# Kernel optimization log

Hardware: AMD Instinct MI355X
Metric: run time of the kernel (lower is better)

## Reference

```python
import jax, jax.numpy as jnp
import numpy as np

N = 100000
E = 1600000
D_IN = 64
D_HID = 64
D_OUT = 64
R = 8
BN_EPS = 1e-5


def setup_inputs() -> dict:
    key = jax.random.key(0)
    ks = jax.random.split(key, 12)
    x = jax.random.normal(ks[0], (N, D_IN), dtype=jnp.float32)
    edge_index = jax.random.randint(ks[1], (2, E), 0, N, dtype=jnp.int64)
    edge_type = jax.random.randint(ks[2], (E,), 0, R, dtype=jnp.int64)
    s1 = 1.0 / np.sqrt(D_IN)
    s2 = 1.0 / np.sqrt(D_HID)
    w1 = jax.random.uniform(ks[3], (R, D_IN, D_HID), jnp.float32, -s1, s1)
    root1 = jax.random.uniform(ks[4], (D_IN, D_HID), jnp.float32, -s1, s1)
    b1 = jnp.zeros((D_HID,), jnp.float32)
    gamma1 = jnp.ones((D_HID,), jnp.float32)
    beta1 = jnp.zeros((D_HID,), jnp.float32)
    w2 = jax.random.uniform(ks[5], (R, D_HID, D_OUT), jnp.float32, -s2, s2)
    root2 = jax.random.uniform(ks[6], (D_HID, D_OUT), jnp.float32, -s2, s2)
    b2 = jnp.zeros((D_OUT,), jnp.float32)
    return {"x": x, "edge_index": edge_index, "edge_type": edge_type,
            "w1": w1, "root1": root1, "b1": b1, "gamma1": gamma1, "beta1": beta1,
            "w2": w2, "root2": root2, "b2": b2}


def rgcn_conv(x, edge_index, edge_type, W, root, bias):
    # PyG RGCNConv with aggr='mean': per relation r, mean of neighbor features
    # over incoming edges of type r, transformed by W[r]; plus root transform + bias.
    # Aggregate-then-transform (legal since transform is linear): one fused
    # segment_sum keyed by (dst, relation), then a grouped GEMM via einsum.
    n, d = x.shape
    src, dst = edge_index[0], edge_index[1]
    seg = dst * R + edge_type                     # [E] combined segment id
    msg = x[src]                                  # [E, d] gather
    agg = jax.ops.segment_sum(msg, seg, num_segments=n * R).reshape(n, R, d)
    cnt = jax.ops.segment_sum(jnp.ones((src.shape[0],), x.dtype), seg,
                              num_segments=n * R).reshape(n, R, 1)
    mean = agg / jnp.maximum(cnt, 1.0)            # [n, R, d]
    return jnp.einsum('nrd,rdo->no', mean, W) + x @ root + bias


def batch_norm(h, gamma, beta):
    mu = h.mean(axis=0)
    var = h.var(axis=0)
    return gamma * (h - mu) * jax.lax.rsqrt(var + BN_EPS) + beta


def reference(x, edge_index, edge_type, w1, root1, b1, gamma1, beta1, w2, root2, b2):
    h = rgcn_conv(x, edge_index, edge_type, w1, root1, b1)
    h = jax.nn.relu(batch_norm(h, gamma1, beta1))
    # dropout: identity (eval mode)
    out = rgcn_conv(h, edge_index, edge_type, w2, root2, b2)
    return out
```

## Files before the change

### kernel.cpp

```cpp
#include <hip/hip_runtime.h>
#include <hip/hip_bf16.h>

#define NN 100000
#define EE 1600000
#define RR 8
#define DD 64
#define MM (NN * RR)
#define BN_EPS 1e-5f
#define KTOT 576
#define BSTRIDE 584

#define NB 391
#define EPB 8192
#define NBIN ((EE + EPB - 1) / EPB)

typedef __bf16 bf16x8 __attribute__((ext_vector_type(8)));
typedef float  f32x4  __attribute__((ext_vector_type(4)));

static __device__ __forceinline__ unsigned short f32_to_bf16(float f) {
    unsigned int u = __float_as_uint(f);
    unsigned int r = u + 0x7FFFu + ((u >> 16) & 1u);
    return (unsigned short)(r >> 16);
}
static __device__ __forceinline__ float bflo(unsigned int u) {
    return __uint_as_float(u << 16);
}
static __device__ __forceinline__ float bfhi(unsigned int u) {
    return __uint_as_float(u & 0xFFFF0000u);
}


__global__ void k_bcount(const int* __restrict__ dst, int* __restrict__ btot) {
    __shared__ int cnt[NB];
    int t = threadIdx.x;
    for (int i = t; i < NB; i += 256) cnt[i] = 0;
    __syncthreads();
    int base = blockIdx.x * EPB;
#pragma unroll
    for (int i = 0; i < EPB / 256; ++i) {
        int e = base + i * 256 + t;
        if (e < EE) atomicAdd(&cnt[dst[e] >> 8], 1);
    }
    __syncthreads();
    for (int i = t; i < NB; i += 256)
        if (cnt[i]) atomicAdd(&btot[i], cnt[i]);
}

__global__ void k_bscan(const int* __restrict__ btot, int* __restrict__ bbase,
                        int* __restrict__ gcur, int* __restrict__ rowptr) {
    __shared__ int sd[512];
    int t = threadIdx.x;
    int v = (t < NB) ? btot[t] : 0;
    sd[t] = v;
    __syncthreads();
    for (int off = 1; off < 512; off <<= 1) {
        int x = (t >= off) ? sd[t - off] : 0;
        __syncthreads();
        sd[t] += x;
        __syncthreads();
    }
    if (t < NB) { bbase[t] = sd[t] - v; gcur[t] = sd[t] - v; }
    if (t == NB - 1) { bbase[NB] = sd[t]; rowptr[MM] = sd[t]; }
}

__global__ void k_bin(const int* __restrict__ src, const int* __restrict__ dst,
                      const int* __restrict__ et, int* __restrict__ gcur,
                      unsigned int* __restrict__ ebuf) {
    __shared__ int cnt[NB];
    __shared__ int bas[NB];
    __shared__ int off[NB];
    int t = threadIdx.x;
    for (int i = t; i < NB; i += 256) { cnt[i] = 0; off[i] = 0; }
    __syncthreads();
    int base = blockIdx.x * EPB;
#pragma unroll
    for (int i = 0; i < EPB / 256; ++i) {
        int e = base + i * 256 + t;
        if (e < EE) atomicAdd(&cnt[dst[e] >> 8], 1);
    }
    __syncthreads();
    for (int i = t; i < NB; i += 256) {
        int c = cnt[i];
        bas[i] = c ? atomicAdd(&gcur[i], c) : 0;
    }
    __syncthreads();
#pragma unroll
    for (int i = 0; i < EPB / 256; ++i) {
        int e = base + i * 256 + t;
        if (e < EE) {
            int d = dst[e];
            int b = d >> 8;
            int lk = ((d & 255) << 3) | et[e];
            unsigned int rec0 = (unsigned int)src[e] | ((unsigned int)lk << 17);
            int p = bas[b] + atomicAdd(&off[b], 1);
            ebuf[p] = rec0;
        }
    }
}

__global__ __launch_bounds__(256) void k_bcsr(const int* __restrict__ bbase,
                                              const unsigned int* __restrict__ ebuf,
                                              int* __restrict__ rowptr,
                                              int* __restrict__ rec) {
    __shared__ int deg[2048];
    __shared__ int part[256];
    int b = blockIdx.x, t = threadIdx.x;
    int e0 = bbase[b], e1 = bbase[b + 1];
    for (int i = t; i < 2048; i += 256) deg[i] = 0;
    __syncthreads();
    for (int e = e0 + t; e < e1; e += 256) atomicAdd(&deg[ebuf[e] >> 17], 1);
    __syncthreads();
    int loc[8];
    int s = 0;
#pragma unroll
    for (int j = 0; j < 8; ++j) { loc[j] = deg[t * 8 + j]; s += loc[j]; }
    part[t] = s;
    __syncthreads();
    for (int off = 1; off < 256; off <<= 1) {
        int x = (t >= off) ? part[t - off] : 0;
        __syncthreads();
        part[t] += x;
        __syncthreads();
    }
    int run = part[t] - s;
    int keyBase = b * 2048;
#pragma unroll
    for (int j = 0; j < 8; ++j) {
        int g = keyBase + t * 8 + j;
        if (g < MM) rowptr[g] = e0 + run;
        deg[t * 8 + j] = run;
        run += loc[j];
    }
    __syncthreads();
    for (int e = e0 + t; e < e1; e += 256) {
        unsigned int v = ebuf[e];
        int lk = v >> 17;
        int pos = e0 + atomicAdd(&deg[lk], 1);
        rec[pos] = (int)(v & 0x1FFFFu);
    }
}


__global__ void k_tobf16(const float* __restrict__ X, unsigned short* __restrict__ Xb) {
    int i = blockIdx.x * 256 + threadIdx.x;
    if (i >= NN * DD / 4) return;
    float4 v = ((const float4*)X)[i];
    ushort4 o;
    o.x = f32_to_bf16(v.x); o.y = f32_to_bf16(v.y);
    o.z = f32_to_bf16(v.z); o.w = f32_to_bf16(v.w);
    ((ushort4*)Xb)[i] = o;
}


__global__ void k_agg(const unsigned short* __restrict__ Xb,
                      const int* __restrict__ rowptr,
                      const int* __restrict__ rec,
                      unsigned short* __restrict__ mean) {
    int wv = threadIdx.x >> 6;
    int lane = threadIdx.x & 63;
    int n = blockIdx.x * 4 + wv;
    if (n >= NN) return;
    int r = lane >> 3;
    int q = lane & 7;
    int e0 = rowptr[n * RR + r];
    int e1 = rowptr[n * RR + r + 1];
    float a0[8] = {0,0,0,0,0,0,0,0};
    float a1[8] = {0,0,0,0,0,0,0,0};
    float a2[8] = {0,0,0,0,0,0,0,0};
    float a3[8] = {0,0,0,0,0,0,0,0};
    int e = e0;
    for (; e + 3 < e1; e += 4) {
        int s0 = rec[e], s1 = rec[e + 1], s2 = rec[e + 2], s3 = rec[e + 3];
        uint4 u0 = *(const uint4*)(Xb + (size_t)s0 * DD + q * 8);
        uint4 u1 = *(const uint4*)(Xb + (size_t)s1 * DD + q * 8);
        uint4 u2 = *(const uint4*)(Xb + (size_t)s2 * DD + q * 8);
        uint4 u3 = *(const uint4*)(Xb + (size_t)s3 * DD + q * 8);
        a0[0] += bflo(u0.x); a0[1] += bfhi(u0.x); a0[2] += bflo(u0.y); a0[3] += bfhi(u0.y);
        a0[4] += bflo(u0.z); a0[5] += bfhi(u0.z); a0[6] += bflo(u0.w); a0[7] += bfhi(u0.w);
        a1[0] += bflo(u1.x); a1[1] += bfhi(u1.x); a1[2] += bflo(u1.y); a1[3] += bfhi(u1.y);
        a1[4] += bflo(u1.z); a1[5] += bfhi(u1.z); a1[6] += bflo(u1.w); a1[7] += bfhi(u1.w);
        a2[0] += bflo(u2.x); a2[1] += bfhi(u2.x); a2[2] += bflo(u2.y); a2[3] += bfhi(u2.y);
        a2[4] += bflo(u2.z); a2[5] += bfhi(u2.z); a2[6] += bflo(u2.w); a2[7] += bfhi(u2.w);
        a3[0] += bflo(u3.x); a3[1] += bfhi(u3.x); a3[2] += bflo(u3.y); a3[3] += bfhi(u3.y);
        a3[4] += bflo(u3.z); a3[5] += bfhi(u3.z); a3[6] += bflo(u3.w); a3[7] += bfhi(u3.w);
    }
    if (e + 1 < e1) {
        int s0 = rec[e], s1 = rec[e + 1];
        uint4 u0 = *(const uint4*)(Xb + (size_t)s0 * DD + q * 8);
        uint4 u1 = *(const uint4*)(Xb + (size_t)s1 * DD + q * 8);
        a0[0] += bflo(u0.x); a0[1] += bfhi(u0.x); a0[2] += bflo(u0.y); a0[3] += bfhi(u0.y);
        a0[4] += bflo(u0.z); a0[5] += bfhi(u0.z); a0[6] += bflo(u0.w); a0[7] += bfhi(u0.w);
        a1[0] += bflo(u1.x); a1[1] += bfhi(u1.x); a1[2] += bflo(u1.y); a1[3] += bfhi(u1.y);
        a1[4] += bflo(u1.z); a1[5] += bfhi(u1.z); a1[6] += bflo(u1.w); a1[7] += bfhi(u1.w);
        e += 2;
    }
    if (e < e1) {
        int s0 = rec[e];
        uint4 u0 = *(const uint4*)(Xb + (size_t)s0 * DD + q * 8);
        a0[0] += bflo(u0.x); a0[1] += bfhi(u0.x); a0[2] += bflo(u0.y); a0[3] += bfhi(u0.y);
        a0[4] += bflo(u0.z); a0[5] += bfhi(u0.z); a0[6] += bflo(u0.w); a0[7] += bfhi(u0.w);
    }
    int cnt = e1 - e0;
    float inv = 1.0f / (float)(cnt > 1 ? cnt : 1);
    uint4 o;
    o.x = (unsigned)f32_to_bf16((a0[0]+a1[0]+a2[0]+a3[0]) * inv) | ((unsigned)f32_to_bf16((a0[1]+a1[1]+a2[1]+a3[1]) * inv) << 16);
    o.y = (unsigned)f32_to_bf16((a0[2]+a1[2]+a2[2]+a3[2]) * inv) | ((unsigned)f32_to_bf16((a0[3]+a1[3]+a2[3]+a3[3]) * inv) << 16);
    o.z = (unsigned)f32_to_bf16((a0[4]+a1[4]+a2[4]+a3[4]) * inv) | ((unsigned)f32_to_bf16((a0[5]+a1[5]+a2[5]+a3[5]) * inv) << 16);
    o.w = (unsigned)f32_to_bf16((a0[6]+a1[6]+a2[6]+a3[6]) * inv) | ((unsigned)f32_to_bf16((a0[7]+a1[7]+a2[7]+a3[7]) * inv) << 16);
    *(uint4*)(mean + (size_t)n * 512 + r * 64 + q * 8) = o;
}


__global__ void k_prepw(const float* __restrict__ W, const float* __restrict__ Root,
                        unsigned short* __restrict__ WcT) {
    int i = blockIdx.x * 256 + threadIdx.x;
    if (i >= 64 * KTOT) return;
    int o = i / KTOT;
    int k = i - o * KTOT;
    float v;
    if (k < 512) v = W[(size_t)(k >> 6) * 4096 + (k & 63) * 64 + o];
    else         v = Root[(k - 512) * 64 + o];
    WcT[(size_t)o * KTOT + k] = f32_to_bf16(v);
}


__global__ __launch_bounds__(256) void k_gemm(const unsigned short* __restrict__ meanB,
                                              const unsigned short* __restrict__ Xb,
                                              const unsigned short* __restrict__ WcT,
                                              const float* __restrict__ bias,
                                              float* __restrict__ Out,
                                              float* __restrict__ stats,
                                              int dostats) {
    __shared__ unsigned short Bs[64 * BSTRIDE];
    __shared__ float ssum[4][64];
    __shared__ float ssq[4][64];
    int t = threadIdx.x;
#pragma unroll
    for (int i = 0; i < 18; ++i) {
        int idx = i * 256 + t;
        int row = idx / 72;
        int k16 = idx - row * 72;
        uint4 v = *(const uint4*)(WcT + (size_t)row * KTOT + k16 * 8);
        *(uint4*)(Bs + row * BSTRIDE + k16 * 8) = v;
    }
    __syncthreads();

    int wv = t >> 6, lane = t & 63;
    int quad = lane >> 4, m16 = lane & 15;
    int row0 = blockIdx.x * 128 + wv * 32;
    int r0 = row0 + m16;
    int r1 = row0 + 16 + m16;
    bool ok0 = r0 < NN, ok1 = r1 < NN;

    union AU { uint4 u; bf16x8 f; };
    f32x4 acc[2][4];
#pragma unroll
    for (int i = 0; i < 2; ++i)
#pragma unroll
        for (int j = 0; j < 4; ++j) acc[i][j] = (f32x4){0.f, 0.f, 0.f, 0.f};

    const unsigned short* a0p = meanB + (size_t)r0 * 512 + quad * 8;
    const unsigned short* a1p = meanB + (size_t)r1 * 512 + quad * 8;
    const unsigned short* x0p = Xb + (size_t)r0 * DD + quad * 8;
    const unsigned short* x1p = Xb + (size_t)r1 * DD + quad * 8;
    const unsigned short* bs  = Bs + m16 * BSTRIDE + quad * 8;

#pragma unroll
    for (int kb = 0; kb < 16; ++kb) {
        AU av0, av1, bv[4];
        if (ok0) av0.u = *(const uint4*)(a0p + kb * 32); else av0.u = make_uint4(0,0,0,0);
        if (ok1) av1.u = *(const uint4*)(a1p + kb * 32); else av1.u = make_uint4(0,0,0,0);
#pragma unroll
        for (int nt = 0; nt < 4; ++nt)
            bv[nt].u = *(const uint4*)(bs + nt * 16 * BSTRIDE + kb * 32);
#pragma unroll
        for (int nt = 0; nt < 4; ++nt) {
            acc[0][nt] = __builtin_amdgcn_mfma_f32_16x16x32_bf16(av0.f, bv[nt].f, acc[0][nt], 0, 0, 0);
            acc[1][nt] = __builtin_amdgcn_mfma_f32_16x16x32_bf16(av1.f, bv[nt].f, acc[1][nt], 0, 0, 0);
        }
    }
#pragma unroll
    for (int kb = 0; kb < 2; ++kb) {
        AU av0, av1, bv[4];
        if (ok0) av0.u = *(const uint4*)(x0p + kb * 32); else av0.u = make_uint4(0,0,0,0);
        if (ok1) av1.u = *(const uint4*)(x1p + kb * 32); else av1.u = make_uint4(0,0,0,0);
#pragma unroll
        for (int nt = 0; nt < 4; ++nt)
            bv[nt].u = *(const uint4*)(bs + nt * 16 * BSTRIDE + 512 + kb * 32);
#pragma unroll
        for (int nt = 0; nt < 4; ++nt) {
            acc[0][nt] = __builtin_amdgcn_mfma_f32_16x16x32_bf16(av0.f, bv[nt].f, acc[0][nt], 0, 0, 0);
            acc[1][nt] = __builtin_amdgcn_mfma_f32_16x16x32_bf16(av1.f, bv[nt].f, acc[1][nt], 0, 0, 0);
        }
    }

#pragma unroll
    for (int rt = 0; rt < 2; ++rt) {
#pragma unroll
        for (int nt = 0; nt < 4; ++nt) {
            int col = nt * 16 + m16;
            float bb = bias[col];
#pragma unroll
            for (int i = 0; i < 4; ++i) {
                int row = row0 + rt * 16 + quad * 4 + i;
                if (row < NN) Out[(size_t)row * 64 + col] = acc[rt][nt][i] + bb;
            }
        }
    }

    if (dostats) {
#pragma unroll
        for (int nt = 0; nt < 4; ++nt) {
            int col = nt * 16 + m16;
            float bb = bias[col];
            float s = 0.f, sq = 0.f;
#pragma unroll
            for (int rt = 0; rt < 2; ++rt) {
#pragma unroll
                for (int i = 0; i < 4; ++i) {
                    int row = row0 + rt * 16 + quad * 4 + i;
                    if (row < NN) {
                        float v = acc[rt][nt][i] + bb;
                        s += v; sq += v * v;
                    }
                }
            }
            s += __shfl_xor(s, 16); s += __shfl_xor(s, 32);
            sq += __shfl_xor(sq, 16); sq += __shfl_xor(sq, 32);
            if (quad == 0) { ssum[wv][col] = s; ssq[wv][col] = sq; }
        }
        __syncthreads();
        if (t < 128) {
            int col = t & 63;
            if (t < 64) {
                float s = ssum[0][col] + ssum[1][col] + ssum[2][col] + ssum[3][col];
                atomicAdd(&stats[col], s);
            } else {
                float sq = ssq[0][col] + ssq[1][col] + ssq[2][col] + ssq[3][col];
                atomicAdd(&stats[64 + col], sq);
            }
        }
    }
}


__global__ void k_bnrelu(float* __restrict__ H, unsigned short* __restrict__ Hb,
                         const float* __restrict__ stats,
                         const float* __restrict__ gamma, const float* __restrict__ beta) {
    int idx = blockIdx.x * 256 + threadIdx.x;
    const int total = NN * DD / 4;
    if (idx >= total) return;
    int c0 = (idx & 15) * 4;
    float4 v = ((const float4*)H)[idx];
    float inv = 1.0f / (float)NN;
    float4 o;
    {
        float mu = stats[c0 + 0] * inv;
        float var = stats[64 + c0 + 0] * inv - mu * mu;
        float sc = gamma[c0 + 0] * rsqrtf(var + BN_EPS);
        float r = sc * (v.x - mu) + beta[c0 + 0];
        o.x = r > 0.f ? r : 0.f;
    }
    {
        float mu = stats[c0 + 1] * inv;
        float var = stats[64 + c0 + 1] * inv - mu * mu;
        float sc = gamma[c0 + 1] * rsqrtf(var + BN_EPS);
        float r = sc * (v.y - mu) + beta[c0 + 1];
        o.y = r > 0.f ? r : 0.f;
    }
    {
        float mu = stats[c0 + 2] * inv;
        float var = stats[64 + c0 + 2] * inv - mu * mu;
        float sc = gamma[c0 + 2] * rsqrtf(var + BN_EPS);
        float r = sc * (v.z - mu) + beta[c0 + 2];
        o.z = r > 0.f ? r : 0.f;
    }
    {
        float mu = stats[c0 + 3] * inv;
        float var = stats[64 + c0 + 3] * inv - mu * mu;
        float sc = gamma[c0 + 3] * rsqrtf(var + BN_EPS);
        float r = sc * (v.w - mu) + beta[c0 + 3];
        o.w = r > 0.f ? r : 0.f;
    }
    ((float4*)H)[idx] = o;
    ushort4 ob;
    ob.x = f32_to_bf16(o.x); ob.y = f32_to_bf16(o.y);
    ob.z = f32_to_bf16(o.z); ob.w = f32_to_bf16(o.w);
    ((ushort4*)Hb)[idx] = ob;
}


static inline size_t alignup(size_t x) { return (x + 255) & ~(size_t)255; }

extern "C" void kernel_launch(void* const* d_in, const int* in_sizes, int n_in,
                              void* d_out, int out_size, void* d_ws, size_t ws_size,
                              hipStream_t stream) {
    const float* x      = (const float*)d_in[0];
    const int*   eidx   = (const int*)d_in[1];
    const int*   etype  = (const int*)d_in[2];
    const float* w1     = (const float*)d_in[3];
    const float* root1  = (const float*)d_in[4];
    const float* b1     = (const float*)d_in[5];
    const float* gamma1 = (const float*)d_in[6];
    const float* beta1  = (const float*)d_in[7];
    const float* w2     = (const float*)d_in[8];
    const float* root2  = (const float*)d_in[9];
    const float* b2     = (const float*)d_in[10];
    float* out = (float*)d_out;

    const int* src = eidx;
    const int* dst = eidx + EE;

    char* w = (char*)d_ws;
    int* rowptr = (int*)w;            w += alignup((size_t)(MM + 1) * 4);
    int* btot   = (int*)w;            w += alignup(512 * 4);
    int* bbase  = (int*)w;            w += alignup(512 * 4);
    int* gcur   = (int*)w;            w += alignup(512 * 4);
    int* rec    = (int*)w;            w += alignup((size_t)EE * 4);
    unsigned short* mean = (unsigned short*)w; w += alignup((size_t)NN * 512 * 2);
    float* h    = (float*)w;          w += alignup((size_t)NN * DD * 4);
    unsigned short* xhb = (unsigned short*)w; w += alignup((size_t)NN * DD * 2);
    unsigned short* wct1 = (unsigned short*)w; w += alignup((size_t)64 * KTOT * 2);
    unsigned short* wct2 = (unsigned short*)w; w += alignup((size_t)64 * KTOT * 2);
    float* stats = (float*)w;         w += alignup(128 * 4);
    unsigned int* ebuf = (unsigned int*)mean;

    hipMemsetAsync(btot, 0, 512 * 4, stream);
    hipMemsetAsync(stats, 0, 128 * 4, stream);

    k_prepw<<<dim3(144), dim3(256), 0, stream>>>(w1, root1, wct1);
    k_prepw<<<dim3(144), dim3(256), 0, stream>>>(w2, root2, wct2);
    k_tobf16<<<dim3(NN * DD / 4 / 256 + 1), dim3(256), 0, stream>>>(x, xhb);

    k_bcount<<<dim3(NBIN), dim3(256), 0, stream>>>(dst, btot);
    k_bscan<<<dim3(1), dim3(512), 0, stream>>>(btot, bbase, gcur, rowptr);
    k_bin<<<dim3(NBIN), dim3(256), 0, stream>>>(src, dst, etype, gcur, ebuf);
    k_bcsr<<<dim3(NB), dim3(256), 0, stream>>>(bbase, ebuf, rowptr, rec);

    k_agg<<<dim3((NN + 3) / 4), dim3(256), 0, stream>>>(xhb, rowptr, rec, mean);
    k_gemm<<<dim3((NN + 127) / 128), dim3(256), 0, stream>>>(mean, xhb, wct1, b1, h, stats, 1);
    k_bnrelu<<<dim3(NN * DD / 4 / 256), dim3(256), 0, stream>>>(h, xhb, stats, gamma1, beta1);

    k_agg<<<dim3((NN + 3) / 4), dim3(256), 0, stream>>>(xhb, rowptr, rec, mean);
    k_gemm<<<dim3((NN + 127) / 128), dim3(256), 0, stream>>>(mean, xhb, wct2, b2, out, stats, 0);
}
```

Measured before the change: 377.8 us.

## Fuse neighbor aggregation with GEMM via shared-memory A tile

Aggregation and the grouped GEMM are merged into one kernel. Each block builds a 32-node by 576-column bf16 A tile (per-relation means plus root features) in LDS and runs MFMA on it, reading the weights straight from global/L2. This removes the write and re-read of the 100000x512 bf16 mean buffer and one launch per layer. It also drops the redundant fp32 H write in the BN/ReLU kernel. The trade-offs are lower parallelism during the gather (8 nodes serialized per wave) and B operands no longer staged in LDS.

```diff
diff --git a/kernel.cpp b/kernel.cpp
--- a/kernel.cpp
+++ b/kernel.cpp
@@ -149,65 +149,6 @@
     o.x = f32_to_bf16(v.x); o.y = f32_to_bf16(v.y);
     o.z = f32_to_bf16(v.z); o.w = f32_to_bf16(v.w);
     ((ushort4*)Xb)[i] = o;
-}
-
-
-__global__ void k_agg(const unsigned short* __restrict__ Xb,
-                      const int* __restrict__ rowptr,
-                      const int* __restrict__ rec,
-                      unsigned short* __restrict__ mean) {
-    int wv = threadIdx.x >> 6;
-    int lane = threadIdx.x & 63;
-    int n = blockIdx.x * 4 + wv;
-    if (n >= NN) return;
-    int r = lane >> 3;
-    int q = lane & 7;
-    int e0 = rowptr[n * RR + r];
-    int e1 = rowptr[n * RR + r + 1];
-    float a0[8] = {0,0,0,0,0,0,0,0};
-    float a1[8] = {0,0,0,0,0,0,0,0};
-    float a2[8] = {0,0,0,0,0,0,0,0};
-    float a3[8] = {0,0,0,0,0,0,0,0};
-    int e = e0;
-    for (; e + 3 < e1; e += 4) {
-        int s0 = rec[e], s1 = rec[e + 1], s2 = rec[e + 2], s3 = rec[e + 3];
-        uint4 u0 = *(const uint4*)(Xb + (size_t)s0 * DD + q * 8);
-        uint4 u1 = *(const uint4*)(Xb + (size_t)s1 * DD + q * 8);
-        uint4 u2 = *(const uint4*)(Xb + (size_t)s2 * DD + q * 8);
-        uint4 u3 = *(const uint4*)(Xb + (size_t)s3 * DD + q * 8);
-        a0[0] += bflo(u0.x); a0[1] += bfhi(u0.x); a0[2] += bflo(u0.y); a0[3] += bfhi(u0.y);
-        a0[4] += bflo(u0.z); a0[5] += bfhi(u0.z); a0[6] += bflo(u0.w); a0[7] += bfhi(u0.w);
-        a1[0] += bflo(u1.x); a1[1] += bfhi(u1.x); a1[2] += bflo(u1.y); a1[3] += bfhi(u1.y);
-        a1[4] += bflo(u1.z); a1[5] += bfhi(u1.z); a1[6] += bflo(u1.w); a1[7] += bfhi(u1.w);
-        a2[0] += bflo(u2.x); a2[1] += bfhi(u2.x); a2[2] += bflo(u2.y); a2[3] += bfhi(u2.y);
-        a2[4] += bflo(u2.z); a2[5] += bfhi(u2.z); a2[6] += bflo(u2.w); a2[7] += bfhi(u2.w);
-        a3[0] += bflo(u3.x); a3[1] += bfhi(u3.x); a3[2] += bflo(u3.y); a3[3] += bfhi(u3.y);
-        a3[4] += bflo(u3.z); a3[5] += bfhi(u3.z); a3[6] += bflo(u3.w); a3[7] += bfhi(u3.w);
-    }
-    if (e + 1 < e1) {
-        int s0 = rec[e], s1 = rec[e + 1];
-        uint4 u0 = *(const uint4*)(Xb + (size_t)s0 * DD + q * 8);
-        uint4 u1 = *(const uint4*)(Xb + (size_t)s1 * DD + q * 8);
-        a0[0] += bflo(u0.x); a0[1] += bfhi(u0.x); a0[2] += bflo(u0.y); a0[3] += bfhi(u0.y);
-        a0[4] += bflo(u0.z); a0[5] += bfhi(u0.z); a0[6] += bflo(u0.w); a0[7] += bfhi(u0.w);
-        a1[0] += bflo(u1.x); a1[1] += bfhi(u1.x); a1[2] += bflo(u1.y); a1[3] += bfhi(u1.y);
-        a1[4] += bflo(u1.z); a1[5] += bfhi(u1.z); a1[6] += bflo(u1.w); a1[7] += bfhi(u1.w);
-        e += 2;
-    }
-    if (e < e1) {
-        int s0 = rec[e];
-        uint4 u0 = *(const uint4*)(Xb + (size_t)s0 * DD + q * 8);
-        a0[0] += bflo(u0.x); a0[1] += bfhi(u0.x); a0[2] += bflo(u0.y); a0[3] += bfhi(u0.y);
-        a0[4] += bflo(u0.z); a0[5] += bfhi(u0.z); a0[6] += bflo(u0.w); a0[7] += bfhi(u0.w);
-    }
-    int cnt = e1 - e0;
-    float inv = 1.0f / (float)(cnt > 1 ? cnt : 1);
-    uint4 o;
-    o.x = (unsigned)f32_to_bf16((a0[0]+a1[0]+a2[0]+a3[0]) * inv) | ((unsigned)f32_to_bf16((a0[1]+a1[1]+a2[1]+a3[1]) * inv) << 16);
-    o.y = (unsigned)f32_to_bf16((a0[2]+a1[2]+a2[2]+a3[2]) * inv) | ((unsigned)f32_to_bf16((a0[3]+a1[3]+a2[3]+a3[3]) * inv) << 16);
-    o.z = (unsigned)f32_to_bf16((a0[4]+a1[4]+a2[4]+a3[4]) * inv) | ((unsigned)f32_to_bf16((a0[5]+a1[5]+a2[5]+a3[5]) * inv) << 16);
-    o.w = (unsigned)f32_to_bf16((a0[6]+a1[6]+a2[6]+a3[6]) * inv) | ((unsigned)f32_to_bf16((a0[7]+a1[7]+a2[7]+a3[7]) * inv) << 16);
-    *(uint4*)(mean + (size_t)n * 512 + r * 64 + q * 8) = o;
 }
 
 
@@ -224,127 +165,134 @@
 }
 
 
-__global__ __launch_bounds__(256) void k_gemm(const unsigned short* __restrict__ meanB,
-                                              const unsigned short* __restrict__ Xb,
-                                              const unsigned short* __restrict__ WcT,
-                                              const float* __restrict__ bias,
-                                              float* __restrict__ Out,
-                                              float* __restrict__ stats,
-                                              int dostats) {
-    __shared__ unsigned short Bs[64 * BSTRIDE];
-    __shared__ float ssum[4][64];
-    __shared__ float ssq[4][64];
+__global__ __launch_bounds__(256, 4) void k_fused(const unsigned short* __restrict__ Xb,
+                                                  const int* __restrict__ rowptr,
+                                                  const int* __restrict__ rec,
+                                                  const unsigned short* __restrict__ WcT,
+                                                  const float* __restrict__ bias,
+                                                  float* __restrict__ Out,
+                                                  float* __restrict__ stats,
+                                                  int dostats) {
+    __shared__ unsigned short Atile[32 * BSTRIDE];
+    __shared__ float ssum[4][32];
+    __shared__ float ssq[4][32];
     int t = threadIdx.x;
-#pragma unroll
-    for (int i = 0; i < 18; ++i) {
-        int idx = i * 256 + t;
-        int row = idx / 72;
-        int k16 = idx - row * 72;
-        uint4 v = *(const uint4*)(WcT + (size_t)row * KTOT + k16 * 8);
-        *(uint4*)(Bs + row * BSTRIDE + k16 * 8) = v;
-    }
-    __syncthreads();
-
     int wv = t >> 6, lane = t & 63;
-    int quad = lane >> 4, m16 = lane & 15;
-    int row0 = blockIdx.x * 128 + wv * 32;
-    int r0 = row0 + m16;
-    int r1 = row0 + 16 + m16;
-    bool ok0 = r0 < NN, ok1 = r1 < NN;
-
+    int r = lane >> 3;
+    int q = lane & 7;
+    int nodeBase = blockIdx.x * 32 + wv * 8;
+    int base8 = nodeBase * RR;
+    int v0 = rowptr[base8 + lane];
+    int v1 = rowptr[base8 + lane + 1];
+
+    {
+        int i = lane >> 3, c = lane & 7;
+        uint4 xv = *(const uint4*)(Xb + (size_t)(nodeBase + i) * DD + c * 8);
+        *(uint4*)(Atile + (size_t)(wv * 8 + i) * BSTRIDE + 512 + c * 8) = xv;
+    }
+
+#pragma unroll 1
+    for (int i = 0; i < 8; ++i) {
+        int e0 = __shfl(v0, i * 8 + r);
+        int e1 = __shfl(v1, i * 8 + r);
+        float a0[8] = {0,0,0,0,0,0,0,0};
+        float a1[8] = {0,0,0,0,0,0,0,0};
+        float a2[8] = {0,0,0,0,0,0,0,0};
+        float a3[8] = {0,0,0,0,0,0,0,0};
+        int e = e0;
+        for (; e + 3 < e1; e += 4) {
+            int s0 = rec[e], s1 = rec[e + 1], s2 = rec[e + 2], s3 = rec[e + 3];
+            uint4 u0 = *(const uint4*)(Xb + (size_t)s0 * DD + q * 8);
+            uint4 u1 = *(const uint4*)(Xb + (size_t)s1 * DD + q * 8);
+            uint4 u2 = *(const uint4*)(Xb + (size_t)s2 * DD + q * 8);
+            uint4 u3 = *(const uint4*)(Xb + (size_t)s3 * DD + q * 8);
+            a0[0] += bflo(u0.x); a0[1] += bfhi(u0.x); a0[2] += bflo(u0.y); a0[3] += bfhi(u0.y);
+            a0[4] += bflo(u0.z); a0[5] += bfhi(u0.z); a0[6] += bflo(u0.w); a0[7] += bfhi(u0.w);
+            a1[0] += bflo(u1.x); a1[1] += bfhi(u1.x); a1[2] += bflo(u1.y); a1[3] += bfhi(u1.y);
+            a1[4] += bflo(u1.z); a1[5] += bfhi(u1.z); a1[6] += bflo(u1.w); a1[7] += bfhi(u1.w);
+            a2[0] += bflo(u2.x); a2[1] += bfhi(u2.x); a2[2] += bflo(u2.y); a2[3] += bfhi(u2.y);
+            a2[4] += bflo(u2.z); a2[5] += bfhi(u2.z); a2[6] += bflo(u2.w); a2[7] += bfhi(u2.w);
+            a3[0] += bflo(u3.x); a3[1] += bfhi(u3.x); a3[2] += bflo(u3.y); a3[3] += bfhi(u3.y);
+            a3[4] += bflo(u3.z); a3[5] += bfhi(u3.z); a3[6] += bflo(u3.w); a3[7] += bfhi(u3.w);
+        }
+        if (e + 1 < e1) {
+            int s0 = rec[e], s1 = rec[e + 1];
+            uint4 u0 = *(const uint4*)(Xb + (size_t)s0 * DD + q * 8);
+            uint4 u1 = *(const uint4*)(Xb + (size_t)s1 * DD + q * 8);
+            a0[0] += bflo(u0.x); a0[1] += bfhi(u0.x); a0[2] += bflo(u0.y); a0[3] += bfhi(u0.y);
+            a0[4] += bflo(u0.z); a0[5] += bfhi(u0.z); a0[6] += bflo(u0.w); a0[7] += bfhi(u0.w);
+            a1[0] += bflo(u1.x); a1[1] += bfhi(u1.x); a1[2] += bflo(u1.y); a1[3] += bfhi(u1.y);
+            a1[4] += bflo(u1.z); a1[5] += bfhi(u1.z); a1[6] += bflo(u1.w); a1[7] += bfhi(u1.w);
+            e += 2;
+        }
+        if (e < e1) {
+            int s0 = rec[e];
+            uint4 u0 = *(const uint4*)(Xb + (size_t)s0 * DD + q * 8);
+            a0[0] += bflo(u0.x); a0[1] += bfhi(u0.x); a0[2] += bflo(u0.y); a0[3] += bfhi(u0.y);
+            a0[4] += bflo(u0.z); a0[5] += bfhi(u0.z); a0[6] += bflo(u0.w); a0[7] += bfhi(u0.w);
+        }
+        int cnt = e1 - e0;
+        float inv = 1.0f / (float)(cnt > 1 ? cnt : 1);
+        uint4 o;
+        o.x = (unsigned)f32_to_bf16((a0[0]+a1[0]+a2[0]+a3[0]) * inv) | ((unsigned)f32_to_bf16((a0[1]+a1[1]+a2[1]+a3[1]) * inv) << 16);
+        o.y = (unsigned)f32_to_bf16((a0[2]+a1[2]+a2[2]+a3[2]) * inv) | ((unsigned)f32_to_bf16((a0[3]+a1[3]+a2[3]+a3[3]) * inv) << 16);
+        o.z = (unsigned)f32_to_bf16((a0[4]+a1[4]+a2[4]+a3[4]) * inv) | ((unsigned)f32_to_bf16((a0[5]+a1[5]+a2[5]+a3[5]) * inv) << 16);
+        o.w = (unsigned)f32_to_bf16((a0[6]+a1[6]+a2[6]+a3[6]) * inv) | ((unsigned)f32_to_bf16((a0[7]+a1[7]+a2[7]+a3[7]) * inv) << 16);
+        *(uint4*)(Atile + (size_t)(wv * 8 + i) * BSTRIDE + lane * 8) = o;
+    }
+    __syncthreads();
+
+    int m16 = lane & 15, quad = lane >> 4;
+    int rt = wv >> 1, ch = wv & 1;
+    const unsigned short* as = Atile + (rt * 16 + m16) * BSTRIDE + quad * 8;
+    const unsigned short* bg = WcT + (size_t)(ch * 32 + m16) * KTOT + quad * 8;
     union AU { uint4 u; bf16x8 f; };
-    f32x4 acc[2][4];
-#pragma unroll
-    for (int i = 0; i < 2; ++i)
-#pragma unroll
-        for (int j = 0; j < 4; ++j) acc[i][j] = (f32x4){0.f, 0.f, 0.f, 0.f};
-
-    const unsigned short* a0p = meanB + (size_t)r0 * 512 + quad * 8;
-    const unsigned short* a1p = meanB + (size_t)r1 * 512 + quad * 8;
-    const unsigned short* x0p = Xb + (size_t)r0 * DD + quad * 8;
-    const unsigned short* x1p = Xb + (size_t)r1 * DD + quad * 8;
-    const unsigned short* bs  = Bs + m16 * BSTRIDE + quad * 8;
-
-#pragma unroll
-    for (int kb = 0; kb < 16; ++kb) {
-        AU av0, av1, bv[4];
-        if (ok0) av0.u = *(const uint4*)(a0p + kb * 32); else av0.u = make_uint4(0,0,0,0);
-        if (ok1) av1.u = *(const uint4*)(a1p + kb * 32); else av1.u = make_uint4(0,0,0,0);
-#pragma unroll
-        for (int nt = 0; nt < 4; ++nt)
-            bv[nt].u = *(const uint4*)(bs + nt * 16 * BSTRIDE + kb * 32);
-#pragma unroll
-        for (int nt = 0; nt < 4; ++nt) {
-            acc[0][nt] = __builtin_amdgcn_mfma_f32_16x16x32_bf16(av0.f, bv[nt].f, acc[0][nt], 0, 0, 0);
-            acc[1][nt] = __builtin_amdgcn_mfma_f32_16x16x32_bf16(av1.f, bv[nt].f, acc[1][nt], 0, 0, 0);
-        }
-    }
-#pragma unroll
-    for (int kb = 0; kb < 2; ++kb) {
-        AU av0, av1, bv[4];
-        if (ok0) av0.u = *(const uint4*)(x0p + kb * 32); else av0.u = make_uint4(0,0,0,0);
-        if (ok1) av1.u = *(const uint4*)(x1p + kb * 32); else av1.u = make_uint4(0,0,0,0);
-#pragma unroll
-        for (int nt = 0; nt < 4; ++nt)
-            bv[nt].u = *(const uint4*)(bs + nt * 16 * BSTRIDE + 512 + kb * 32);
-#pragma unroll
-        for (int nt = 0; nt < 4; ++nt) {
-            acc[0][nt] = __builtin_amdgcn_mfma_f32_16x16x32_bf16(av0.f, bv[nt].f, acc[0][nt], 0, 0, 0);
-            acc[1][nt] = __builtin_amdgcn_mfma_f32_16x16x32_bf16(av1.f, bv[nt].f, acc[1][nt], 0, 0, 0);
-        }
-    }
-
-#pragma unroll
-    for (int rt = 0; rt < 2; ++rt) {
-#pragma unroll
-        for (int nt = 0; nt < 4; ++nt) {
-            int col = nt * 16 + m16;
-            float bb = bias[col];
-#pragma unroll
-            for (int i = 0; i < 4; ++i) {
-                int row = row0 + rt * 16 + quad * 4 + i;
-                if (row < NN) Out[(size_t)row * 64 + col] = acc[rt][nt][i] + bb;
-            }
-        }
-    }
-
-    if (dostats) {
-#pragma unroll
-        for (int nt = 0; nt < 4; ++nt) {
-            int col = nt * 16 + m16;
-            float bb = bias[col];
-            float s = 0.f, sq = 0.f;
-#pragma unroll
-            for (int rt = 0; rt < 2; ++rt) {
-#pragma unroll
-                for (int i = 0; i < 4; ++i) {
-                    int row = row0 + rt * 16 + quad * 4 + i;
-                    if (row < NN) {
-                        float v = acc[rt][nt][i] + bb;
-                        s += v; sq += v * v;
-                    }
-                }
-            }
+    f32x4 acc[2];
+    acc[0] = (f32x4){0.f, 0.f, 0.f, 0.f};
+    acc[1] = (f32x4){0.f, 0.f, 0.f, 0.f};
+#pragma unroll
+    for (int kb = 0; kb < 18; ++kb) {
+        AU av, b0, b1;
+        av.u = *(const uint4*)(as + kb * 32);
+        b0.u = *(const uint4*)(bg + kb * 32);
+        b1.u = *(const uint4*)(bg + 16 * KTOT + kb * 32);
+        acc[0] = __builtin_amdgcn_mfma_f32_16x16x32_bf16(av.f, b0.f, acc[0], 0, 0, 0);
+        acc[1] = __builtin_amdgcn_mfma_f32_16x16x32_bf16(av.f, b1.f, acc[1], 0, 0, 0);
+    }
+
+    int row0 = blockIdx.x * 32 + rt * 16 + quad * 4;
+#pragma unroll
+    for (int nt = 0; nt < 2; ++nt) {
+        int col = ch * 32 + nt * 16 + m16;
+        float bb = bias[col];
+        float s = 0.f, sq = 0.f;
+#pragma unroll
+        for (int i2 = 0; i2 < 4; ++i2) {
+            float v = acc[nt][i2] + bb;
+            Out[(size_t)(row0 + i2) * 64 + col] = v;
+            s += v; sq += v * v;
+        }
+        if (dostats) {
             s += __shfl_xor(s, 16); s += __shfl_xor(s, 32);
             sq += __shfl_xor(sq, 16); sq += __shfl_xor(sq, 32);
-            if (quad == 0) { ssum[wv][col] = s; ssq[wv][col] = sq; }
-        }
-        __syncthreads();
-        if (t < 128) {
-            int col = t & 63;
-            if (t < 64) {
-                float s = ssum[0][col] + ssum[1][col] + ssum[2][col] + ssum[3][col];
-                atomicAdd(&stats[col], s);
-            } else {
-                float sq = ssq[0][col] + ssq[1][col] + ssq[2][col] + ssq[3][col];
-                atomicAdd(&stats[64 + col], sq);
-            }
-        }
-    }
-}
-
-
-__global__ void k_bnrelu(float* __restrict__ H, unsigned short* __restrict__ Hb,
+            if (quad == 0) { ssum[wv][nt * 16 + m16] = s; ssq[wv][nt * 16 + m16] = sq; }
+        }
+    }
+    if (dostats) {
+        __syncthreads();
+        if (t < 64) {
+            int half = t >> 5, cl = t & 31;
+            atomicAdd(&stats[t], ssum[half][cl] + ssum[half + 2][cl]);
+        } else if (t < 128) {
+            int c2 = t - 64;
+            int half = c2 >> 5, cl = c2 & 31;
+            atomicAdd(&stats[64 + c2], ssq[half][cl] + ssq[half + 2][cl]);
+        }
+    }
+}
+
+
+__global__ void k_bnrelu(const float* __restrict__ H, unsigned short* __restrict__ Hb,
                          const float* __restrict__ stats,
                          const float* __restrict__ gamma, const float* __restrict__ beta) {
     int idx = blockIdx.x * 256 + threadIdx.x;
@@ -382,7 +330,6 @@
         float r = sc * (v.w - mu) + beta[c0 + 3];
         o.w = r > 0.f ? r : 0.f;
     }
-    ((float4*)H)[idx] = o;
     ushort4 ob;
     ob.x = f32_to_bf16(o.x); ob.y = f32_to_bf16(o.y);
     ob.z = f32_to_bf16(o.z); ob.w = f32_to_bf16(o.w);
@@ -417,13 +364,12 @@
     int* bbase  = (int*)w;            w += alignup(512 * 4);
     int* gcur   = (int*)w;            w += alignup(512 * 4);
     int* rec    = (int*)w;            w += alignup((size_t)EE * 4);
-    unsigned short* mean = (unsigned short*)w; w += alignup((size_t)NN * 512 * 2);
     float* h    = (float*)w;          w += alignup((size_t)NN * DD * 4);
     unsigned short* xhb = (unsigned short*)w; w += alignup((size_t)NN * DD * 2);
     unsigned short* wct1 = (unsigned short*)w; w += alignup((size_t)64 * KTOT * 2);
     unsigned short* wct2 = (unsigned short*)w; w += alignup((size_t)64 * KTOT * 2);
     float* stats = (float*)w;         w += alignup(128 * 4);
-    unsigned int* ebuf = (unsigned int*)mean;
+    unsigned int* ebuf = (unsigned int*)h;
 
     hipMemsetAsync(btot, 0, 512 * 4, stream);
     hipMemsetAsync(stats, 0, 128 * 4, stream);
@@ -437,10 +383,8 @@
     k_bin<<<dim3(NBIN), dim3(256), 0, stream>>>(src, dst, etype, gcur, ebuf);
     k_bcsr<<<dim3(NB), dim3(256), 0, stream>>>(bbase, ebuf, rowptr, rec);
 
-    k_agg<<<dim3((NN + 3) / 4), dim3(256), 0, stream>>>(xhb, rowptr, rec, mean);
-    k_gemm<<<dim3((NN + 127) / 128), dim3(256), 0, stream>>>(mean, xhb, wct1, b1, h, stats, 1);
+    k_fused<<<dim3(NN / 32), dim3(256), 0, stream>>>(xhb, rowptr, rec, wct1, b1, h, stats, 1);
     k_bnrelu<<<dim3(NN * DD / 4 / 256), dim3(256), 0, stream>>>(h, xhb, stats, gamma1, beta1);
 
-    k_agg<<<dim3((NN + 3) / 4), dim3(256), 0, stream>>>(xhb, rowptr, rec, mean);
-    k_gemm<<<dim3((NN + 127) / 128), dim3(256), 0, stream>>>(mean, xhb, wct2, b2, out, stats, 0);
-}
+    k_fused<<<dim3(NN / 32), dim3(256), 0, stream>>>(xhb, rowptr, rec, wct2, b2, out, stats, 0);
+}
```

After: 451.6 us. 1.2x slower.
